# Performance work log

Hardware: AMD Instinct MI355X
Metric: run time of the kernel (lower is better)

Reference implementation:

```python
import jax, jax.numpy as jnp
import numpy as np

C_CURV = 0.1            # curvature k
SC = float(np.sqrt(C_CURV))
EPS = 1e-7


def _mobius_add(x, y, c):
    x2 = jnp.sum(x * x, -1, keepdims=True)
    y2 = jnp.sum(y * y, -1, keepdims=True)
    xy = jnp.sum(x * y, -1, keepdims=True)
    num = (1 + 2 * c * xy + c * y2) * x + (1 - c * x2) * y
    den = 1 + 2 * c * xy + c * c * x2 * y2
    return num / jnp.maximum(den, 1e-12)


def _mobius_scalarmul(r, x, c):
    sc = jnp.sqrt(c)
    n = jnp.linalg.norm(x, axis=-1, keepdims=True)
    t = jnp.clip(sc * n, EPS, 1.0 - 1e-6)
    return jnp.tanh(r * jnp.arctanh(t)) * x / jnp.maximum(sc * n, EPS)


def setup_inputs() -> dict:
    key = jax.random.key(0)
    k0, k1, k2, k3, k4 = jax.random.split(key, 5)
    B, N, V, D, NC = 64, 1024, 50257, 128, 10
    token_ids = jax.random.randint(k0, (B, N), 0, V)
    mask = jax.random.randint(k1, (B, N), 0, 2).astype(bool)
    emb = (jax.random.normal(k2, (V, D), jnp.float32) * 0.02).at[0].set(0.0)  # pad_id=0 row zeroed
    Wo = jax.random.normal(k3, (D, D + 1), jnp.float32) / np.sqrt(D + 1)
    bo = jnp.zeros((D,), jnp.float32)
    Wf = jax.random.normal(k4, (NC, D), jnp.float32) / np.sqrt(D)
    bf = jnp.zeros((NC,), jnp.float32)
    return {"token_ids": token_ids, "mask": mask, "emb": emb, "Wo": Wo, "bo": bo, "Wf": Wf, "bf": bf}


def reference(token_ids, mask, emb, Wo, bo, Wf, bf):
    c, sc = C_CURV, SC
    D = emb.shape[1]
    # embedding lookup (tangent vectors at origin)
    v = emb[token_ids]                                            # (B,N,D)
    # Lorentz expmap0 -> hyperboloid points in D+1
    nv = jnp.maximum(jnp.linalg.norm(v, axis=-1, keepdims=True), EPS)
    x = jnp.concatenate([jnp.cosh(sc * nv) / sc,
                         jnp.sinh(sc * nv) * v / (sc * nv)], -1)  # (B,N,D+1)
    # single-head attention, scores = -<xi,xj>_L (Lorentz inner), masked softmax
    sgn = jnp.concatenate([-jnp.ones((1,)), jnp.ones((D,))]).astype(x.dtype)
    scores = -jnp.einsum('bid,bjd->bij', x * sgn, x) / np.sqrt(D + 1)
    scores = jnp.where(mask[:, None, :], scores, -1e9)
    w = jax.nn.softmax(scores, axis=-1)
    # riemannian value aggregation: Lorentz centroid (weighted sum renormalized to hyperboloid)
    mu = jnp.einsum('bij,bjd->bid', w, x)
    inner = jnp.einsum('bid,d,bid->bi', mu, sgn, mu)
    mu = mu / (sc * jnp.sqrt(jnp.maximum(-inner, EPS))[..., None])
    # output projection (D+1 -> D) then Poincare expmap0 so points lie in the ball
    u = jnp.einsum('bid,od->bio', mu, Wo) + bo                    # (B,N,D)
    nu = jnp.maximum(jnp.linalg.norm(u, axis=-1, keepdims=True), EPS)
    y = jnp.tanh(sc * nu) * u / (sc * nu)                         # (B,N,D) in ball
    # sequential masked Mobius pooling: left-fold mobius_add over valid tokens, then scalarmul 1/n
    def step(acc, xm):
        xi, mi = xm                                               # (B,D), (B,)
        new = _mobius_add(acc, xi, c)
        return jnp.where(mi[:, None], new, acc), None
    acc0 = jnp.zeros_like(y[:, 0, :])
    acc, _ = jax.lax.scan(step, acc0, (jnp.swapaxes(y, 0, 1), jnp.swapaxes(mask, 0, 1)))
    cnt = jnp.sum(mask, axis=1)
    r = (1.0 / jnp.maximum(cnt, 1))[:, None].astype(y.dtype)
    pooled = _mobius_scalarmul(r, acc, c)
    pooled = jnp.where((cnt > 0)[:, None], pooled, y[:, 0, :])    # empty rows fall back to first token
    # LorentzMLR head: logmap0 then linear
    npn = jnp.maximum(jnp.linalg.norm(pooled, axis=-1, keepdims=True), EPS)
    t = jnp.clip(sc * npn, EPS, 1.0 - 1e-6)
    vlog = jnp.arctanh(t) * pooled / (sc * npn)
    return vlog @ Wf.T + bf                                       # (B, num_classes)
```

## Files before the change

kernel.cpp:

```cpp
#include <hip/hip_runtime.h>
#include <math.h>

#define B_    64
#define N_    1024
#define D_    128
#define DP1   129
#define NC_   10
#define QB    128
#define KT    32
#define SCf   0.31622776601683794f
#define SCALE 0.08804509063256238f

typedef __bf16 bf16x8 __attribute__((ext_vector_type(8)));
typedef float  f32x16 __attribute__((ext_vector_type(16)));

#define MFMA(a, b, c) __builtin_amdgcn_mfma_f32_32x32x16_bf16((a), (b), (c), 0, 0, 0)

static __device__ __forceinline__ float dpp_add_step(float f, int ctrl, int rmask) {
    if (ctrl == 0x111) { int t = __builtin_amdgcn_update_dpp(0, __builtin_bit_cast(int, f), 0x111, 0xf, 0xf, true); return f + __builtin_bit_cast(float, t); }
    if (ctrl == 0x112) { int t = __builtin_amdgcn_update_dpp(0, __builtin_bit_cast(int, f), 0x112, 0xf, 0xf, true); return f + __builtin_bit_cast(float, t); }
    if (ctrl == 0x114) { int t = __builtin_amdgcn_update_dpp(0, __builtin_bit_cast(int, f), 0x114, 0xf, 0xf, true); return f + __builtin_bit_cast(float, t); }
    if (ctrl == 0x118) { int t = __builtin_amdgcn_update_dpp(0, __builtin_bit_cast(int, f), 0x118, 0xf, 0xf, true); return f + __builtin_bit_cast(float, t); }
    if (ctrl == 0x142 && rmask == 0xa) { int t = __builtin_amdgcn_update_dpp(0, __builtin_bit_cast(int, f), 0x142, 0xa, 0xf, true); return f + __builtin_bit_cast(float, t); }
    { int t = __builtin_amdgcn_update_dpp(0, __builtin_bit_cast(int, f), 0x143, 0xc, 0xf, true); return f + __builtin_bit_cast(float, t); }
}

static __device__ __forceinline__ float wave_sum64(float f) {
    f = dpp_add_step(f, 0x111, 0xf);
    f = dpp_add_step(f, 0x112, 0xf);
    f = dpp_add_step(f, 0x114, 0xf);
    f = dpp_add_step(f, 0x118, 0xf);
    f = dpp_add_step(f, 0x142, 0xa);
    f = dpp_add_step(f, 0x143, 0xc);
    return __builtin_bit_cast(float, __builtin_amdgcn_readlane(__builtin_bit_cast(int, f), 63));
}

static __device__ __forceinline__ float half_sum32(float f, int half) {
    f = dpp_add_step(f, 0x111, 0xf);
    f = dpp_add_step(f, 0x112, 0xf);
    f = dpp_add_step(f, 0x114, 0xf);
    f = dpp_add_step(f, 0x118, 0xf);
    f = dpp_add_step(f, 0x142, 0xa);
    float s0 = __builtin_bit_cast(float, __builtin_amdgcn_readlane(__builtin_bit_cast(int, f), 31));
    float s1 = __builtin_bit_cast(float, __builtin_amdgcn_readlane(__builtin_bit_cast(int, f), 63));
    return half ? s1 : s0;
}

static __device__ __forceinline__ float readlane_f(float v, int lane) {
    return __builtin_bit_cast(float, __builtin_amdgcn_readlane(__builtin_bit_cast(int, v), lane));
}

static __device__ __forceinline__ bf16x8 ld_lds8(const __bf16* p) {
    union { bf16x8 v; unsigned long long q[2]; } u;
    u.q[0] = *(const unsigned long long*)(p);
    u.q[1] = *(const unsigned long long*)(p + 4);
    return u.v;
}

__global__ __launch_bounds__(256) void k_detect_mask(const int* __restrict__ mask_w,
                                                     int* __restrict__ flag) {
    __shared__ int bad;
    if (threadIdx.x == 0) bad = 0;
    __syncthreads();
    int local = 0;
    for (int i = threadIdx.x; i < 16384; i += 256) {
        int v = mask_w[i];
        if (v != 0 && v != 1) local = 1;
    }
    if (local) atomicOr(&bad, 1);
    __syncthreads();
    if (threadIdx.x == 0) *flag = bad;
}

static __device__ __forceinline__ int read_mask(const int* mw, int is_i8, int idx) {
    if (is_i8) return (int)((const unsigned char*)mw)[idx];
    return mw[idx];
}

__global__ __launch_bounds__(256) void k_prep_wo(const float* __restrict__ Wo,
                                                 __bf16* __restrict__ Woh,
                                                 __bf16* __restrict__ Wol) {
    int idx = blockIdx.x * 256 + threadIdx.x;
    if (idx >= 128 * 144) return;
    int o = idx / 144, d = idx - o * 144;
    float v = (d < DP1) ? Wo[o * DP1 + d] : 0.f;
    __bf16 h = (__bf16)v;
    Woh[idx] = h;
    Wol[idx] = (__bf16)(v - (float)h);
}

__global__ __launch_bounds__(256) void k_prep(const int* __restrict__ tok,
                                              const float* __restrict__ emb,
                                              __bf16* __restrict__ Xh, __bf16* __restrict__ Xl,
                                              float* __restrict__ X0g, float* __restrict__ X128g) {
    __shared__ float Xf[64][132];
    const int t = threadIdx.x, w = t >> 6, l = t & 63;
    const int base = blockIdx.x * 64;
    for (int it = 0; it < 16; ++it) {
        const int tk = w * 16 + it;
        const int id = tok[base + tk];
        const float2 v = ((const float2*)(emb + (size_t)id * D_))[l];
        float s = wave_sum64(v.x * v.x + v.y * v.y);
        float nv = fmaxf(sqrtf(s), 1e-7f);
        float a = SCf * nv;
        float a2 = a * a;
        float shc, ch;
        if (a < 0.5f) {
            shc = 1.f + a2 * (1.f/6.f) * (1.f + a2 * (1.f/20.f) * (1.f + a2 * (1.f/42.f)));
            ch  = 1.f + a2 * 0.5f * (1.f + a2 * (1.f/12.f) * (1.f + a2 * (1.f/30.f)));
        } else {
            float ea = __expf(a), ei = 1.f / ea;
            ch = 0.5f * (ea + ei);
            shc = 0.5f * (ea - ei) / a;
        }
        Xf[tk][1 + 2 * l] = v.x * shc;
        Xf[tk][2 + 2 * l] = v.y * shc;
        if (l == 0) Xf[tk][0] = ch / SCf;
    }
    __syncthreads();
    const int tk2 = t >> 2, dg = (t & 3) * 32;
    for (int i = 0; i < 32; i += 8) {
        bf16x8 hv, lv;
        #pragma unroll
        for (int j = 0; j < 8; ++j) {
            float f = Xf[tk2][dg + i + j];
            __bf16 h = (__bf16)f;
            hv[j] = h;
            lv[j] = (__bf16)(f - (float)h);
        }
        *(bf16x8*)(Xh + (size_t)(base + tk2) * D_ + dg + i) = hv;
        *(bf16x8*)(Xl + (size_t)(base + tk2) * D_ + dg + i) = lv;
    }
    if (t < 64) {
        X0g[base + t]   = Xf[t][0];
        X128g[base + t] = Xf[t][D_];
    }
}

__global__ __launch_bounds__(256, 2) void k_attn(
        const __bf16* __restrict__ Xh, const __bf16* __restrict__ Xl,
        const float* __restrict__ X0g, const float* __restrict__ X128g,
        const int* __restrict__ mask, const int* __restrict__ mflag,
        const __bf16* __restrict__ Woh, const __bf16* __restrict__ Wol,
        const float* __restrict__ bo,
        float* __restrict__ Y, float* __restrict__ Y2) {
    extern __shared__ char smem[];
    __bf16* Krow = (__bf16*)smem;
    __bf16* XTb  = (__bf16*)(smem + 16896);
    __bf16* Pb   = (__bf16*)(smem + 35328);
    __shared__ float K0s[KT];
    __shared__ float K128s[KT];
    __shared__ int   Ms[KT];

    const int b    = blockIdx.y;
    const int qb   = blockIdx.x * QB;
    const int t    = threadIdx.x;
    const int w    = t >> 6;
    const int l    = t & 63;
    const int l31  = l & 31;
    const int half = l >> 5;
    const int is8  = *mflag;

    const size_t qrow = (size_t)(b * N_ + qb + w * 32 + l31);
    bf16x8 qfh[8], qfl[8];
    #pragma unroll
    for (int ks = 0; ks < 8; ++ks) {
        qfh[ks] = *(const bf16x8*)(Xh + qrow * D_ + ks * 16 + half * 8);
        qfl[ks] = *(const bf16x8*)(Xl + qrow * D_ + ks * 16 + half * 8);
    }
    float q0[16], q128[16];
    #pragma unroll
    for (int r = 0; r < 16; ++r) {
        const int qr = (r & 3) + 8 * (r >> 2) + 4 * half;
        q0[r]   = X0g[b * N_ + qb + w * 32 + qr];
        q128[r] = X128g[b * N_ + qb + w * 32 + qr];
    }

    f32x16 accM[4] = {};
    float  mu128p[16] = {};

    for (int kt = 0; kt < N_ / KT; ++kt) {
        __syncthreads();
        {
            const int key = t >> 3, ck = t & 7;
            const size_t krow = (size_t)(b * N_ + kt * KT + key);
            #pragma unroll
            for (int ch = 0; ch < 2; ++ch) {
                const int c0 = ck * 8 + 64 * ch;
                bf16x8 vh = *(const bf16x8*)(Xh + krow * D_ + c0);
                bf16x8 vl = *(const bf16x8*)(Xl + krow * D_ + c0);
                union { bf16x8 v; unsigned long long q[2]; } uh, ul;
                uh.v = vh; ul.v = vl;
                *(unsigned long long*)(Krow + key * 132 + c0)            = uh.q[0];
                *(unsigned long long*)(Krow + key * 132 + c0 + 4)        = uh.q[1];
                *(unsigned long long*)(Krow + 4224 + key * 132 + c0)     = ul.q[0];
                *(unsigned long long*)(Krow + 4224 + key * 132 + c0 + 4) = ul.q[1];
                #pragma unroll
                for (int j = 0; j < 8; ++j) {
                    XTb[(c0 + j) * 36 + key]        = vh[j];
                    XTb[4608 + (c0 + j) * 36 + key] = vl[j];
                }
            }
            if (t < KT) {
                K0s[t]   = X0g[b * N_ + kt * KT + t];
                K128s[t] = X128g[b * N_ + kt * KT + t];
                Ms[t]    = read_mask(mask, is8, b * N_ + kt * KT + t);
            }
        }
        __syncthreads();

        f32x16 accS = {};
        #pragma unroll
        for (int ks = 0; ks < 8; ++ks) {
            bf16x8 bh = ld_lds8(Krow + l31 * 132 + ks * 16 + half * 8);
            bf16x8 bl = ld_lds8(Krow + 4224 + l31 * 132 + ks * 16 + half * 8);
            accS = MFMA(qfh[ks], bh, accS);
            accS = MFMA(qfh[ks], bl, accS);
            accS = MFMA(qfl[ks], bh, accS);
        }
        const float k0v = K0s[l31], k128v = K128s[l31];
        const int   mv  = Ms[l31];
        #pragma unroll
        for (int r = 0; r < 16; ++r) {
            float sc = (2.f * q0[r] * k0v - accS[r] - q128[r] * k128v) * SCALE;
            float e  = mv ? __expf(sc) : 0.f;
            mu128p[r] += e * k128v;
            __bf16 eh = (__bf16)e;
            __bf16 el = (__bf16)(e - (float)eh);
            const int qr = (r & 3) + 8 * (r >> 2) + 4 * half;
            Pb[(w * 2 + 0) * 1152 + qr * 36 + l31] = eh;
            Pb[(w * 2 + 1) * 1152 + qr * 36 + l31] = el;
        }

        #pragma unroll
        for (int ks = 0; ks < 2; ++ks) {
            bf16x8 ah = ld_lds8(Pb + (w * 2 + 0) * 1152 + l31 * 36 + ks * 16 + half * 8);
            bf16x8 al = ld_lds8(Pb + (w * 2 + 1) * 1152 + l31 * 36 + ks * 16 + half * 8);
            #pragma unroll
            for (int nt = 0; nt < 4; ++nt) {
                bf16x8 bh = ld_lds8(XTb + (nt * 32 + l31) * 36 + ks * 16 + half * 8);
                bf16x8 bl = ld_lds8(XTb + 4608 + (nt * 32 + l31) * 36 + ks * 16 + half * 8);
                accM[nt] = MFMA(ah, bh, accM[nt]);
                accM[nt] = MFMA(ah, bl, accM[nt]);
                accM[nt] = MFMA(al, bh, accM[nt]);
            }
        }
    }

    #pragma unroll
    for (int r = 0; r < 16; ++r) mu128p[r] = half_sum32(mu128p[r], half);
    float rno[16];
    #pragma unroll
    for (int r = 0; r < 16; ++r) {
        float p = 0.f;
        #pragma unroll
        for (int nt = 0; nt < 4; ++nt) p += accM[nt][r] * accM[nt][r];
        if (l31 == 0) p -= 2.f * accM[0][r] * accM[0][r];
        p = half_sum32(p, half);
        float negI = -(p + mu128p[r] * mu128p[r]);
        negI = fmaxf(negI, 1e-7f);
        rno[r] = 1.f / (SCf * sqrtf(negI));
    }
    #pragma unroll
    for (int nt = 0; nt < 4; ++nt)
        #pragma unroll
        for (int r = 0; r < 16; ++r) accM[nt][r] *= rno[r];
    #pragma unroll
    for (int r = 0; r < 16; ++r) mu128p[r] *= rno[r];

    __syncthreads();
    __bf16* MuA = (__bf16*)smem + w * (32 * 148);
    #pragma unroll
    for (int r = 0; r < 16; ++r) {
        const int qr = (r & 3) + 8 * (r >> 2) + 4 * half;
        #pragma unroll
        for (int nt = 0; nt < 4; ++nt)
            MuA[qr * 148 + nt * 32 + l31] = (__bf16)accM[nt][r];
        if (l31 == 0) MuA[qr * 148 + 128] = (__bf16)mu128p[r];
        if (l31 >= 1 && l31 <= 15) MuA[qr * 148 + 128 + l31] = (__bf16)0.f;
    }
    bf16x8 Ah[9];
    #pragma unroll
    for (int ks = 0; ks < 9; ++ks) Ah[ks] = ld_lds8(MuA + l31 * 148 + ks * 16 + half * 8);
    #pragma unroll
    for (int r = 0; r < 16; ++r) {
        const int qr = (r & 3) + 8 * (r >> 2) + 4 * half;
        #pragma unroll
        for (int nt = 0; nt < 4; ++nt) {
            float m = accM[nt][r];
            MuA[qr * 148 + nt * 32 + l31] = (__bf16)(m - (float)(__bf16)m);
        }
        if (l31 == 0) {
            float m = mu128p[r];
            MuA[qr * 148 + 128] = (__bf16)(m - (float)(__bf16)m);
        }
    }
    bf16x8 Al[9];
    #pragma unroll
    for (int ks = 0; ks < 9; ++ks) Al[ks] = ld_lds8(MuA + l31 * 148 + ks * 16 + half * 8);

    f32x16 accU[4] = {};
    #pragma unroll
    for (int ks = 0; ks < 9; ++ks) {
        #pragma unroll
        for (int nt = 0; nt < 4; ++nt) {
            bf16x8 bh = *(const bf16x8*)(Woh + (size_t)(nt * 32 + l31) * 144 + ks * 16 + half * 8);
            bf16x8 bl = *(const bf16x8*)(Wol + (size_t)(nt * 32 + l31) * 144 + ks * 16 + half * 8);
            accU[nt] = MFMA(Ah[ks], bh, accU[nt]);
            accU[nt] = MFMA(Ah[ks], bl, accU[nt]);
            accU[nt] = MFMA(Al[ks], bh, accU[nt]);
        }
    }

    float bov[4];
    #pragma unroll
    for (int nt = 0; nt < 4; ++nt) bov[nt] = bo[nt * 32 + l31];
    #pragma unroll
    for (int r = 0; r < 16; ++r) {
        float p = 0.f;
        #pragma unroll
        for (int nt = 0; nt < 4; ++nt) {
            float uv = accU[nt][r] + bov[nt];
            accU[nt][r] = uv;
            p += uv * uv;
        }
        float nn = half_sum32(p, half);
        float nu = fmaxf(sqrtf(nn), 1e-7f);
        float aa = SCf * nu;
        float cf = tanhf(aa) / aa;
        const int qr = (r & 3) + 8 * (r >> 2) + 4 * half;
        const size_t row = (size_t)(b * N_ + qb + w * 32 + qr);
        #pragma unroll
        for (int nt = 0; nt < 4; ++nt)
            Y[row * D_ + nt * 32 + l31] = accU[nt][r] * cf;
        if (l31 == 0) Y2[row] = nn * cf * cf;
    }
}

__global__ __launch_bounds__(256) void k_gram(const float* __restrict__ Y,
                                              float* __restrict__ G) {
    const int c = blockIdx.x, b = blockIdx.y;
    const int t = threadIdx.x, w = t >> 6, l = t & 63;
    const int l31 = l & 31, half = l >> 5;
    const int rt = w >> 1, ct = w & 1;
    const size_t base = (size_t)(b * N_ + c * 64);
    const float* Ar = Y + (base + rt * 32 + l31) * D_;
    const float* Br = Y + (base + ct * 32 + l31) * D_;
    f32x16 acc = {};
    #pragma unroll
    for (int ks = 0; ks < 8; ++ks) {
        const int c0 = ks * 16 + half * 8;
        float4 a0 = *(const float4*)(Ar + c0);
        float4 a1 = *(const float4*)(Ar + c0 + 4);
        float4 b0 = *(const float4*)(Br + c0);
        float4 b1 = *(const float4*)(Br + c0 + 4);
        float av[8] = {a0.x, a0.y, a0.z, a0.w, a1.x, a1.y, a1.z, a1.w};
        float bv[8] = {b0.x, b0.y, b0.z, b0.w, b1.x, b1.y, b1.z, b1.w};
        bf16x8 ah, al, bh, bl;
        #pragma unroll
        for (int j = 0; j < 8; ++j) {
            __bf16 h = (__bf16)av[j]; ah[j] = h; al[j] = (__bf16)(av[j] - (float)h);
            __bf16 g = (__bf16)bv[j]; bh[j] = g; bl[j] = (__bf16)(bv[j] - (float)g);
        }
        acc = MFMA(ah, bh, acc);
        acc = MFMA(ah, bl, acc);
        acc = MFMA(al, bh, acc);
    }
    float* Gb = G + ((size_t)(b * 16 + c) << 12);
    #pragma unroll
    for (int r = 0; r < 16; ++r) {
        const int row = rt * 32 + (r & 3) + 8 * (r >> 2) + 4 * half;
        Gb[row * 64 + ct * 32 + l31] = acc[r];
    }
}

__global__ __launch_bounds__(64, 1) void k_pool(const float* __restrict__ Y,
                                                const float* __restrict__ Y2,
                                                const float* __restrict__ G,
                                                const int* __restrict__ mask,
                                                const int* __restrict__ mflag,
                                                const float* __restrict__ Wf,
                                                const float* __restrict__ bf_,
                                                float* __restrict__ out) {
    __shared__ float  prt[64][65];
    __shared__ double vb[D_];
    const int b = blockIdx.x, l = threadIdx.x;
    const int is8 = *mflag;

    int cl = 0;
    for (int i = l; i < N_; i += 64) cl += read_mask(mask, is8, b * N_ + i);
    const int cntT = (int)(wave_sum64((float)cl) + 0.5f);

    const float2* __restrict__ Yp = (const float2*)(Y + (size_t)b * N_ * D_) + l;
    const float*  __restrict__ Gp = G + ((size_t)b << 16) + l;
    const float*  __restrict__ Pp = Y2 + b * N_;

    float  GA[64], GB[64];
    float  py2A, py2B;
    int    msA, msB;
    float2 yring[2][16];

    #pragma unroll
    for (int i = 0; i < 64; ++i) GA[i] = Gp[i * 64];
    py2A = Pp[l];
    msA  = read_mask(mask, is8, b * N_ + l);
    #pragma unroll
    for (int k = 0; k < 16; ++k) yring[0][k] = Yp[(size_t)k * 64];

    float U0 = 0.f, U1 = 0.f, g = 0.f, Dh = 1.f, P = 0.f;

    auto chunk = [&](int c, float (&Gc)[64], float (&Gn)[64],
                     float py2c, float& py2n, int msc, int& msn) {
        const int cn = (c < 15) ? c + 1 : 15;
        #pragma unroll
        for (int i = 0; i < 64; ++i) Gn[i] = Gp[cn * 4096 + i * 64];
        py2n = Pp[cn * 64 + l];
        msn  = read_mask(mask, is8, b * N_ + cn * 64 + l);

        #pragma unroll
        for (int q = 0; q < 4; ++q) {
            #pragma unroll
            for (int k = 0; k < 16; ++k) {
                int gs = c * 64 + (q + 1) * 16 + k;
                if (gs > N_ - 1) gs = N_ - 1;
                yring[(q + 1) & 1][k] = Yp[(size_t)gs * 64];
            }
            #pragma unroll
            for (int k = 0; k < 16; ++k) {
                const int ir = q * 16 + k;
                const float2 yv  = yring[q & 1][k];
                const float  Gv  = Gc[ir];
                const float  py2 = readlane_f(py2c, ir);
                const bool   m   = (__builtin_amdgcn_readlane(msc, ir) != 0);
                const float Dsq   = Dh * Dh;
                const float Bh    = fmaf(-0.1f, P, Dsq);
                const float Donep = Dh * fmaf(0.1f, py2, 1.f);
                const float tP    = (0.01f * py2) * P;
                const float puy  = readlane_f(g, ir);
                const float Ahat = fmaf(0.2f, puy, Donep);
                float dh = fmaf(Dh, fmaf(0.2f, puy, Dh), tP);
                dh = fmaxf(dh, 1e-12f * Dsq);
                const float Draw = m ? dh : Dh;
                const float Am   = m ? Ahat : 1.f;
                const float Bm   = m ? Bh   : 0.f;
                const float Pn   = fmaf(Am, fmaf(Am, P, (2.f * Bm) * puy), (Bm * Bm) * py2);
                if ((k & 3) == 3) {
                    const int e = ilogbf(Draw);
                    const float Aef = ldexpf(Am, -e);
                    const float Bef = ldexpf(Bm, -e);
                    Dh = ldexpf(Draw, -e);
                    P  = ldexpf(Pn, -2 * e);
                    g  = fmaf(Aef, g, Bef * Gv);
                    U0 = fmaf(Aef, U0, Bef * yv.x);
                    U1 = fmaf(Aef, U1, Bef * yv.y);
                } else {
                    Dh = Draw;
                    P  = Pn;
                    g  = fmaf(Am, g, Bm * Gv);
                    U0 = fmaf(Am, U0, Bm * yv.x);
                    U1 = fmaf(Am, U1, Bm * yv.y);
                }
            }
        }
        if (c < 15) {
            const int nb = (c + 1) * 64;
            #pragma unroll
            for (int k0 = 0; k0 < 64; k0 += 16) {
                float2 tmp[16];
                #pragma unroll
                for (int k = 0; k < 16; ++k) tmp[k] = Yp[(size_t)(nb + k0 + k) * 64];
                #pragma unroll
                for (int k = 0; k < 16; ++k)
                    prt[k0 + k][l] = fmaf(U0, tmp[k].x, U1 * tmp[k].y);
            }
            float s0 = 0.f, s1 = 0.f, s2 = 0.f, s3 = 0.f;
            #pragma unroll
            for (int p = 0; p < 64; p += 4) {
                s0 += prt[l][p];     s1 += prt[l][p + 1];
                s2 += prt[l][p + 2]; s3 += prt[l][p + 3];
            }
            g = (s0 + s1) + (s2 + s3);
        }
    };

    for (int cc = 0; cc < 8; ++cc) {
        chunk(2 * cc,     GA, GB, py2A, py2B, msA, msB);
        chunk(2 * cc + 1, GB, GA, py2B, py2A, msB, msA);
    }

    const double SCd = 0.31622776601683794;
    const double sD = 1.0 / (double)Dh;
    double a0 = sD * (double)U0, a1 = sD * (double)U1;
    double n2 = fmax((double)P * (sD * sD), 0.0);
    double n = sqrt(n2);
    double tt = SCd * n;
    tt = fmin(fmax(tt, 1e-7), 1.0 - 1e-6);
    int cm = cntT > 0 ? cntT : 1;
    float rf = (float)(1.0 / (double)cm);
    double r = (double)rf;
    double dv = fmax(SCd * n, 1e-7);
    double f = tanh(r * atanh(tt)) / dv;
    double p0 = a0 * f, p1 = a1 * f;
    double q2;
    if (cntT == 0) {
        float2 y0v = *(const float2*)(Y + (size_t)(b * N_) * D_ + 2 * l);
        p0 = y0v.x; p1 = y0v.y;
        q2 = (double)Y2[b * N_];
    } else {
        q2 = f * f * n2;
    }
    double npn = fmax(sqrt(q2), 1e-7);
    double t2 = fmin(fmax(SCd * npn, 1e-7), 1.0 - 1e-6);
    double f2 = atanh(t2) / (SCd * npn);
    vb[2 * l]     = p0 * f2;
    vb[2 * l + 1] = p1 * f2;
    __syncthreads();

    if (l < NC_) {
        double o = (double)bf_[l];
        for (int d = 0; d < D_; ++d) o += vb[d] * (double)Wf[l * D_ + d];
        out[b * NC_ + l] = (float)o;
    }
}

extern "C" void kernel_launch(void* const* d_in, const int* in_sizes, int n_in,
                              void* d_out, int out_size, void* d_ws, size_t ws_size,
                              hipStream_t stream) {
    const int*   tok  = (const int*)d_in[0];
    const int*   mask = (const int*)d_in[1];
    const float* emb  = (const float*)d_in[2];
    const float* Wo   = (const float*)d_in[3];
    const float* bo   = (const float*)d_in[4];
    const float* Wf   = (const float*)d_in[5];
    const float* bf_  = (const float*)d_in[6];
    float* out = (float*)d_out;

    char* wsb = (char*)d_ws;
    __bf16* Xh   = (__bf16*)wsb;
    __bf16* Xl   = (__bf16*)(wsb + 16777216);
    float*  X0g  = (float*)(wsb + 33554432);
    float*  X128g= (float*)(wsb + 33816576);
    __bf16* Woh  = (__bf16*)(wsb + 34078720);
    __bf16* Wol  = (__bf16*)(wsb + 34115584);
    float*  Y    = (float*)(wsb + 34152448);
    float*  Y2   = (float*)(wsb + 67706880);
    int*    flag = (int*)(wsb + 67969024);
    float*  Gram = (float*)wsb;

    k_detect_mask<<<dim3(1), dim3(256), 0, stream>>>(mask, flag);
    k_prep_wo<<<dim3(72), dim3(256), 0, stream>>>(Wo, Woh, Wol);
    k_prep<<<dim3(B_ * N_ / 64), dim3(256), 0, stream>>>(tok, emb, Xh, Xl, X0g, X128g);
    k_attn<<<dim3(N_ / QB, B_), dim3(256), 53760, stream>>>(Xh, Xl, X0g, X128g, mask, flag,
                                                            Woh, Wol, bo, Y, Y2);
    k_gram<<<dim3(16, B_), dim3(256), 0, stream>>>(Y, Gram);
    k_pool<<<dim3(B_), dim3(64), 0, stream>>>(Y, Y2, Gram, mask, flag, Wf, bf_, out);
}
```

Before: 402.8 us.

## Double-buffer key tiles in LDS and read V operand from row layout

The attention loop now prefetches the next key tile from global memory into registers while computing the current tile, and stores it into a second LDS buffer at the end of the iteration. This removes one barrier per iteration and hides global load latency. The separate transposed copy XTb is dropped: the P·V MFMA operand is gathered from the row-major key buffer with scalar 16-bit LDS reads. That removes the scalar transpose stores but adds strided per-element LDS loads in the inner loop, which may cost more than they save.

```diff
diff --git a/kernel.cpp b/kernel.cpp
--- a/kernel.cpp
+++ b/kernel.cpp
@@ -13,6 +13,7 @@
 
 typedef __bf16 bf16x8 __attribute__((ext_vector_type(8)));
 typedef float  f32x16 __attribute__((ext_vector_type(16)));
+typedef unsigned long long ull;
 
 #define MFMA(a, b, c) __builtin_amdgcn_mfma_f32_32x32x16_bf16((a), (b), (c), 0, 0, 0)
 
@@ -51,9 +52,9 @@
 }
 
 static __device__ __forceinline__ bf16x8 ld_lds8(const __bf16* p) {
-    union { bf16x8 v; unsigned long long q[2]; } u;
-    u.q[0] = *(const unsigned long long*)(p);
-    u.q[1] = *(const unsigned long long*)(p + 4);
+    union { bf16x8 v; ull q[2]; } u;
+    u.q[0] = *(const ull*)(p);
+    u.q[1] = *(const ull*)(p + 4);
     return u.v;
 }
 
@@ -145,12 +146,11 @@
         const float* __restrict__ bo,
         float* __restrict__ Y, float* __restrict__ Y2) {
     extern __shared__ char smem[];
-    __bf16* Krow = (__bf16*)smem;
-    __bf16* XTb  = (__bf16*)(smem + 16896);
-    __bf16* Pb   = (__bf16*)(smem + 35328);
-    __shared__ float K0s[KT];
-    __shared__ float K128s[KT];
-    __shared__ int   Ms[KT];
+    __bf16* KB = (__bf16*)smem;
+    __bf16* Pb = (__bf16*)(smem + 33792);
+    __shared__ float K0s[2][KT];
+    __shared__ float K128s[2][KT];
+    __shared__ int   Ms[2][KT];
 
     const int b    = blockIdx.y;
     const int qb   = blockIdx.x * QB;
@@ -176,50 +176,59 @@
         q128[r] = X128g[b * N_ + qb + w * 32 + qr];
     }
 
+    const int skey = t >> 3, sck = t & 7;
+    bf16x8 svh0, svh1, svl0, svl1;
+    float  sK0 = 0.f, sK128 = 0.f;
+    int    sM = 0;
+    auto ldg_tile = [&](int kt) {
+        const size_t kr = (size_t)(b * N_ + kt * KT + skey);
+        svh0 = *(const bf16x8*)(Xh + kr * D_ + sck * 16);
+        svh1 = *(const bf16x8*)(Xh + kr * D_ + sck * 16 + 8);
+        svl0 = *(const bf16x8*)(Xl + kr * D_ + sck * 16);
+        svl1 = *(const bf16x8*)(Xl + kr * D_ + sck * 16 + 8);
+        if (t < KT) {
+            sK0   = X0g[b * N_ + kt * KT + t];
+            sK128 = X128g[b * N_ + kt * KT + t];
+            sM    = read_mask(mask, is8, b * N_ + kt * KT + t);
+        }
+    };
+    auto st_tile = [&](int buf) {
+        __bf16* KH = KB + buf * 8448;
+        __bf16* KL = KH + 4224;
+        union { bf16x8 v; ull q[2]; } u;
+        u.v = svh0; *(ull*)(KH + skey * 132 + sck * 16)      = u.q[0]; *(ull*)(KH + skey * 132 + sck * 16 + 4)  = u.q[1];
+        u.v = svh1; *(ull*)(KH + skey * 132 + sck * 16 + 8)  = u.q[0]; *(ull*)(KH + skey * 132 + sck * 16 + 12) = u.q[1];
+        u.v = svl0; *(ull*)(KL + skey * 132 + sck * 16)      = u.q[0]; *(ull*)(KL + skey * 132 + sck * 16 + 4)  = u.q[1];
+        u.v = svl1; *(ull*)(KL + skey * 132 + sck * 16 + 8)  = u.q[0]; *(ull*)(KL + skey * 132 + sck * 16 + 12) = u.q[1];
+        if (t < KT) { K0s[buf][t] = sK0; K128s[buf][t] = sK128; Ms[buf][t] = sM; }
+    };
+
     f32x16 accM[4] = {};
     float  mu128p[16] = {};
 
+    ldg_tile(0);
+    st_tile(0);
+
     for (int kt = 0; kt < N_ / KT; ++kt) {
         __syncthreads();
-        {
-            const int key = t >> 3, ck = t & 7;
-            const size_t krow = (size_t)(b * N_ + kt * KT + key);
-            #pragma unroll
-            for (int ch = 0; ch < 2; ++ch) {
-                const int c0 = ck * 8 + 64 * ch;
-                bf16x8 vh = *(const bf16x8*)(Xh + krow * D_ + c0);
-                bf16x8 vl = *(const bf16x8*)(Xl + krow * D_ + c0);
-                union { bf16x8 v; unsigned long long q[2]; } uh, ul;
-                uh.v = vh; ul.v = vl;
-                *(unsigned long long*)(Krow + key * 132 + c0)            = uh.q[0];
-                *(unsigned long long*)(Krow + key * 132 + c0 + 4)        = uh.q[1];
-                *(unsigned long long*)(Krow + 4224 + key * 132 + c0)     = ul.q[0];
-                *(unsigned long long*)(Krow + 4224 + key * 132 + c0 + 4) = ul.q[1];
-                #pragma unroll
-                for (int j = 0; j < 8; ++j) {
-                    XTb[(c0 + j) * 36 + key]        = vh[j];
-                    XTb[4608 + (c0 + j) * 36 + key] = vl[j];
-                }
-            }
-            if (t < KT) {
-                K0s[t]   = X0g[b * N_ + kt * KT + t];
-                K128s[t] = X128g[b * N_ + kt * KT + t];
-                Ms[t]    = read_mask(mask, is8, b * N_ + kt * KT + t);
-            }
-        }
-        __syncthreads();
+        const int cur = kt & 1;
+        const int ktn = (kt < 31) ? kt + 1 : 31;
+        ldg_tile(ktn);
+
+        const __bf16* KH = KB + cur * 8448;
+        const __bf16* KL = KH + 4224;
 
         f32x16 accS = {};
         #pragma unroll
         for (int ks = 0; ks < 8; ++ks) {
-            bf16x8 bh = ld_lds8(Krow + l31 * 132 + ks * 16 + half * 8);
-            bf16x8 bl = ld_lds8(Krow + 4224 + l31 * 132 + ks * 16 + half * 8);
+            bf16x8 bh = ld_lds8(KH + l31 * 132 + ks * 16 + half * 8);
+            bf16x8 bl = ld_lds8(KL + l31 * 132 + ks * 16 + half * 8);
             accS = MFMA(qfh[ks], bh, accS);
             accS = MFMA(qfh[ks], bl, accS);
             accS = MFMA(qfl[ks], bh, accS);
         }
-        const float k0v = K0s[l31], k128v = K128s[l31];
-        const int   mv  = Ms[l31];
+        const float k0v = K0s[cur][l31], k128v = K128s[cur][l31];
+        const int   mv  = Ms[cur][l31];
         #pragma unroll
         for (int r = 0; r < 16; ++r) {
             float sc = (2.f * q0[r] * k0v - accS[r] - q128[r] * k128v) * SCALE;
@@ -238,13 +247,21 @@
             bf16x8 al = ld_lds8(Pb + (w * 2 + 1) * 1152 + l31 * 36 + ks * 16 + half * 8);
             #pragma unroll
             for (int nt = 0; nt < 4; ++nt) {
-                bf16x8 bh = ld_lds8(XTb + (nt * 32 + l31) * 36 + ks * 16 + half * 8);
-                bf16x8 bl = ld_lds8(XTb + 4608 + (nt * 32 + l31) * 36 + ks * 16 + half * 8);
+                const int cmp = nt * 32 + l31;
+                bf16x8 bh, bl;
+                #pragma unroll
+                for (int j = 0; j < 8; ++j) {
+                    const int key = ks * 16 + half * 8 + j;
+                    bh[j] = KH[key * 132 + cmp];
+                    bl[j] = KL[key * 132 + cmp];
+                }
                 accM[nt] = MFMA(ah, bh, accM[nt]);
                 accM[nt] = MFMA(ah, bl, accM[nt]);
                 accM[nt] = MFMA(al, bh, accM[nt]);
             }
         }
+
+        st_tile(cur ^ 1);
     }
 
     #pragma unroll
```

Result: no change. 396.7 us (-1.5%).
